# Optimization experiments

Measured on AMD Instinct MI355X. Metric: run time of the kernel, lower is better.

Reference implementation:

```python
import jax, jax.numpy as jnp
import numpy as np

B, S, D, H, E = 64, 1024, 1024, 64, 8  # batch, seq, model_dim, bottleneck, num_adapters
EPS = 1e-5


def setup_inputs() -> dict:
    key = jax.random.key(0)
    ks = jax.random.split(key, 8)
    x = jax.random.normal(ks[0], (B, S, D), jnp.float32)
    return {
        "x": x,
        # pre-adapter LayerNorm params
        "ln_g": jnp.ones((D,), jnp.float32),
        "ln_b": jnp.zeros((D,), jnp.float32),
        # router BatchNorm1d (eval mode: running stats)
        "bn_g": jnp.ones((D,), jnp.float32),
        "bn_b": jnp.zeros((D,), jnp.float32),
        "bn_mean": jax.random.normal(ks[1], (D,), jnp.float32) * 0.01,
        "bn_var": jnp.ones((D,), jnp.float32),
        # router linear D -> E
        "Wr": jax.random.normal(ks[2], (D, E), jnp.float32) * 0.02,
        "br": jnp.zeros((E,), jnp.float32),
        # per-expert bottleneck adapter weights
        "W_down": jax.random.normal(ks[3], (E, D, H), jnp.float32) * 0.02,
        "b_down": jnp.zeros((E, H), jnp.float32),
        "W_up": jax.random.normal(ks[4], (E, H, D), jnp.float32) * 0.02,
        "b_up": jnp.zeros((E, D), jnp.float32),
    }


def reference(x, ln_g, ln_b, bn_g, bn_b, bn_mean, bn_var, Wr, br,
              W_down, b_down, W_up, b_up):
    # pre layer norm
    mu = jnp.mean(x, axis=-1, keepdims=True)
    var = jnp.var(x, axis=-1, keepdims=True)
    z = (x - mu) * jax.lax.rsqrt(var + EPS) * ln_g + ln_b  # [B,S,D]

    # sentence embedding -> batchnorm (eval) -> router softmax
    z_sent = jnp.mean(z, axis=1)  # [B,D]
    z_bn = (z_sent - bn_mean) * jax.lax.rsqrt(bn_var + EPS) * bn_g + bn_b
    probs = jax.nn.softmax(z_bn @ Wr + br, axis=-1)  # [B,E]

    # hard top-1 routing; gate = prob of selected expert (SparseDispatcher combine)
    idx = jnp.argmax(probs, axis=-1)  # [B] int
    gate = jnp.take_along_axis(probs, idx[:, None], axis=1)[:, 0]  # [B]

    # per-expert bottleneck adapter, applied via gathered expert weights
    # (mathematically identical to dispatch/per-expert-GEMM/scatter-combine)
    h = jax.nn.relu(jnp.einsum('bsd,bdh->bsh', z, W_down[idx]) + b_down[idx][:, None, :])
    y = jnp.einsum('bsh,bhd->bsd', h, W_up[idx]) + b_up[idx][:, None, :]

    return y * gate[:, None, None]  # weighted combine
```

## Files before the change

### kernel.cpp

```cpp
#include <hip/hip_runtime.h>
#include <hip/hip_bf16.h>

#define B_  64
#define S_  1024
#define D_  1024
#define H_  64
#define E_  8
#define EPS_ 1e-5f

typedef __attribute__((ext_vector_type(8))) __bf16 bf16x8;
typedef __attribute__((ext_vector_type(4))) __bf16 bf16x4;
typedef __attribute__((ext_vector_type(4))) float f32x4;

__global__ __launch_bounds__(256) void swz_kernel(
    const float* __restrict__ Wd, const float* __restrict__ Wu,
    __bf16* __restrict__ wd_swz, __bf16* __restrict__ wu_swz)
{
    int t = blockIdx.x * 256 + threadIdx.x;
    if (t < 65536) {
        int e = t >> 13, rem = t & 8191;
        int ks = rem >> 8, nc = (rem >> 6) & 3, lane = rem & 63;
        int k0 = ks * 32 + (lane >> 4) * 8, n = nc * 16 + (lane & 15);
        bf16x8 o;
#pragma unroll
        for (int j = 0; j < 8; ++j)
            o[j] = (__bf16)Wd[((size_t)e * D_ + k0 + j) * H_ + n];
        *(bf16x8*)(wd_swz + (size_t)t * 8) = o;
    } else {
        int t2 = t - 65536;
        int e = t2 >> 13, rem = t2 & 8191;
        int ks = rem >> 12, nc = (rem >> 6) & 63, lane = rem & 63;
        int k0 = ks * 32 + (lane >> 4) * 8, n = nc * 16 + (lane & 15);
        bf16x8 o;
#pragma unroll
        for (int j = 0; j < 8; ++j)
            o[j] = (__bf16)Wu[((size_t)e * H_ + k0 + j) * D_ + n];
        *(bf16x8*)(wu_swz + (size_t)t2 * 8) = o;
    }
}

__global__ __launch_bounds__(256) void ln_kernel(
    const float* __restrict__ x, const float* __restrict__ ln_g,
    const float* __restrict__ ln_b,
    __bf16* __restrict__ z, float* __restrict__ zpart)
{
    const int lane = threadIdx.x & 63, w = threadIdx.x >> 6;
    const int b = blockIdx.x >> 5, sblk = blockIdx.x & 31;
    __shared__ float accs[D_];
    for (int i = threadIdx.x; i < D_; i += 256) accs[i] = 0.f;
    __syncthreads();

    float part[16];
#pragma unroll
    for (int i = 0; i < 16; ++i) part[i] = 0.f;

    for (int it = 0; it < 8; ++it) {
        int s = sblk * 32 + it * 4 + w;
        const float* xr = x + ((size_t)b * S_ + s) * D_;
        f32x4 v[4];
        float s1 = 0.f, s2 = 0.f;
#pragma unroll
        for (int j = 0; j < 4; ++j) {
            v[j] = *(const f32x4*)(xr + j * 256 + lane * 4);
#pragma unroll
            for (int tt = 0; tt < 4; ++tt) { s1 += v[j][tt]; s2 += v[j][tt] * v[j][tt]; }
        }
#pragma unroll
        for (int o = 32; o; o >>= 1) { s1 += __shfl_xor(s1, o); s2 += __shfl_xor(s2, o); }
        float mu = s1 * (1.f / D_);
        float var = s2 * (1.f / D_) - mu * mu;
        float rs = rsqrtf(var + EPS_);

        __bf16 zb[16];
#pragma unroll
        for (int j = 0; j < 4; ++j) {
            int c0 = j * 256 + lane * 4;
            f32x4 gg = *(const f32x4*)(ln_g + c0);
            f32x4 bb = *(const f32x4*)(ln_b + c0);
#pragma unroll
            for (int tt = 0; tt < 4; ++tt) {
                float zz = (v[j][tt] - mu) * rs * gg[tt] + bb[tt];
                part[j * 4 + tt] += zz;
                zb[j * 4 + tt] = (__bf16)zz;
            }
        }
        __bf16* zr = z + ((size_t)b * S_ + s) * D_;
#pragma unroll
        for (int j = 0; j < 4; ++j)
            *(bf16x4*)(zr + j * 256 + lane * 4) = *(bf16x4*)&zb[j * 4];
    }

#pragma unroll
    for (int j = 0; j < 4; ++j)
#pragma unroll
        for (int tt = 0; tt < 4; ++tt)
            atomicAdd(&accs[j * 256 + lane * 4 + tt], part[j * 4 + tt]);
    __syncthreads();
    float* zp = zpart + ((size_t)b * 32 + sblk) * D_;
    for (int i = threadIdx.x; i < D_; i += 256) zp[i] = accs[i];
}

__global__ __launch_bounds__(256) void router_kernel(
    const float* __restrict__ zpart,
    const float* __restrict__ bn_g, const float* __restrict__ bn_b,
    const float* __restrict__ bn_mean, const float* __restrict__ bn_var,
    const float* __restrict__ Wr, const float* __restrict__ br,
    int* __restrict__ idx, float* __restrict__ gate)
{
    const int b = blockIdx.x, tid = threadIdx.x;
    float acc[E_] = {};
    for (int d = tid; d < D_; d += 256) {
        float s = 0.f;
#pragma unroll
        for (int p = 0; p < 32; ++p) s += zpart[((size_t)b * 32 + p) * D_ + d];
        float zb = (s * (1.f / S_) - bn_mean[d]) * rsqrtf(bn_var[d] + EPS_) * bn_g[d] + bn_b[d];
#pragma unroll
        for (int e = 0; e < E_; ++e) acc[e] += zb * Wr[d * E_ + e];
    }
#pragma unroll
    for (int o = 32; o; o >>= 1)
#pragma unroll
        for (int e = 0; e < E_; ++e) acc[e] += __shfl_xor(acc[e], o);

    __shared__ float red[4][E_];
    int lane = tid & 63, w = tid >> 6;
    if (lane == 0)
#pragma unroll
        for (int e = 0; e < E_; ++e) red[w][e] = acc[e];
    __syncthreads();
    if (tid == 0) {
        float logits[E_];
#pragma unroll
        for (int e = 0; e < E_; ++e)
            logits[e] = red[0][e] + red[1][e] + red[2][e] + red[3][e] + br[e];
        float mx = logits[0]; int am = 0;
#pragma unroll
        for (int e = 1; e < E_; ++e) if (logits[e] > mx) { mx = logits[e]; am = e; }
        float den = 0.f;
#pragma unroll
        for (int e = 0; e < E_; ++e) den += expf(logits[e] - mx);
        idx[b] = am;
        gate[b] = 1.f / den;
    }
}

__global__ __launch_bounds__(256) void adapter_kernel(
    const __bf16* __restrict__ z, const __bf16* __restrict__ wd_swz,
    const __bf16* __restrict__ wu_swz,
    const float* __restrict__ b_down, const float* __restrict__ b_up,
    const int* __restrict__ idx, const float* __restrict__ gate,
    float* __restrict__ out)
{
    const int tid = threadIdx.x, lane = tid & 63, w = tid >> 6;
    const int b = blockIdx.x >> 3, tile = blockIdx.x & 7;
    const int e = idx[b];
    const float g = gate[b];
    const int s0 = tile * 128 + w * 32;
    const int r = lane & 15, kb = lane >> 4;

    f32x4 acc[2][4] = {};
    const __bf16* zrow0 = z + ((size_t)(b * S_ + s0 + r)) * D_ + kb * 8;
    const __bf16* zrow1 = zrow0 + (size_t)16 * D_;
    const __bf16* wdp = wd_swz + ((size_t)e * 32 * 4 * 64 + lane) * 8;
#pragma unroll 4
    for (int ks = 0; ks < 32; ++ks) {
        bf16x8 a0 = *(const bf16x8*)(zrow0 + ks * 32);
        bf16x8 a1 = *(const bf16x8*)(zrow1 + ks * 32);
        const __bf16* wk = wdp + (size_t)ks * (4 * 64 * 8);
#pragma unroll
        for (int nc = 0; nc < 4; ++nc) {
            bf16x8 bf = *(const bf16x8*)(wk + nc * (64 * 8));
            acc[0][nc] = __builtin_amdgcn_mfma_f32_16x16x32_bf16(a0, bf, acc[0][nc], 0, 0, 0);
            acc[1][nc] = __builtin_amdgcn_mfma_f32_16x16x32_bf16(a1, bf, acc[1][nc], 0, 0, 0);
        }
    }

    __shared__ __bf16 hlds[4][32 * 64];
    __bf16* hw = &hlds[w][0];
#pragma unroll
    for (int mr = 0; mr < 2; ++mr)
#pragma unroll
        for (int nc = 0; nc < 4; ++nc)
#pragma unroll
            for (int reg = 0; reg < 4; ++reg) {
                int row = mr * 16 + kb * 4 + reg;
                int col = nc * 16 + r;
                float v = acc[mr][nc][reg] + b_down[e * H_ + col];
                v = fmaxf(v, 0.f);
                int chunk = (col >> 3) ^ (row & 7);
                hw[row * 64 + chunk * 8 + (col & 7)] = (__bf16)v;
            }
    __syncthreads();

    bf16x8 a2[2][2];
#pragma unroll
    for (int mr = 0; mr < 2; ++mr)
#pragma unroll
        for (int ks2 = 0; ks2 < 2; ++ks2) {
            int row = mr * 16 + r;
            int chunk = (ks2 * 4 + kb) ^ (row & 7);
            a2[mr][ks2] = *(const bf16x8*)(hw + row * 64 + chunk * 8);
        }

    const __bf16* wup = wu_swz + ((size_t)e * 2 * 64 * 64 + lane) * 8;
    float* outp = out + ((size_t)(b * S_ + s0)) * D_;
#pragma unroll 2
    for (int nc2 = 0; nc2 < 64; ++nc2) {
        bf16x8 b0 = *(const bf16x8*)(wup + (size_t)(0 * 64 + nc2) * (64 * 8));
        bf16x8 b1 = *(const bf16x8*)(wup + (size_t)(1 * 64 + nc2) * (64 * 8));
        int d = nc2 * 16 + r;
        float bup = b_up[e * D_ + d];
#pragma unroll
        for (int mr = 0; mr < 2; ++mr) {
            f32x4 acy = {};
            acy = __builtin_amdgcn_mfma_f32_16x16x32_bf16(a2[mr][0], b0, acy, 0, 0, 0);
            acy = __builtin_amdgcn_mfma_f32_16x16x32_bf16(a2[mr][1], b1, acy, 0, 0, 0);
#pragma unroll
            for (int reg = 0; reg < 4; ++reg) {
                int row = mr * 16 + kb * 4 + reg;
                outp[(size_t)row * D_ + d] = (acy[reg] + bup) * g;
            }
        }
    }
}

extern "C" void kernel_launch(void* const* d_in, const int* in_sizes, int n_in,
                              void* d_out, int out_size, void* d_ws, size_t ws_size,
                              hipStream_t stream)
{
    const float* x       = (const float*)d_in[0];
    const float* ln_g    = (const float*)d_in[1];
    const float* ln_b    = (const float*)d_in[2];
    const float* bn_g    = (const float*)d_in[3];
    const float* bn_b    = (const float*)d_in[4];
    const float* bn_mean = (const float*)d_in[5];
    const float* bn_var  = (const float*)d_in[6];
    const float* Wr      = (const float*)d_in[7];
    const float* br      = (const float*)d_in[8];
    const float* W_down  = (const float*)d_in[9];
    const float* b_down  = (const float*)d_in[10];
    const float* W_up    = (const float*)d_in[11];
    const float* b_up    = (const float*)d_in[12];
    float* out = (float*)d_out;

    char* ws = (char*)d_ws;
    __bf16* z       = (__bf16*)(ws);
    float*  zpart   = (float*)(ws + 134217728);
    __bf16* wd_swz  = (__bf16*)(ws + 142606336);
    __bf16* wu_swz  = (__bf16*)(ws + 143654912);
    int*    idx     = (int*)(ws + 144703488);
    float*  gate    = (float*)(ws + 144703744);

    swz_kernel<<<dim3(512), dim3(256), 0, stream>>>(W_down, W_up, wd_swz, wu_swz);
    ln_kernel<<<dim3(B_ * 32), dim3(256), 0, stream>>>(x, ln_g, ln_b, z, zpart);
    router_kernel<<<dim3(B_), dim3(256), 0, stream>>>(zpart, bn_g, bn_b, bn_mean,
                                                      bn_var, Wr, br, idx, gate);
    adapter_kernel<<<dim3(B_ * 8), dim3(256), 0, stream>>>(z, wd_swz, wu_swz,
                                                           b_down, b_up, idx, gate, out);
}
```

Measured before the change: 606.3 us.

## Split adapter into down and up kernels with transposed MFMA for vectorized stores

Splits the fused adapter kernel into a down-projection kernel that writes the bf16 bottleneck activations h to global memory, and an up-projection kernel with twice as many blocks. The MFMA operands are swapped (weights as A, activations as B) so each lane holds four consecutive output columns and can issue 16-byte float4 stores instead of scattered scalar stores. The LayerNorm kernel also doubles its grid, with the router summing 64 partial sums instead of 32. This costs an extra launch and a round trip of h (about 8 MB) through global memory.

```diff
diff --git a/kernel.cpp b/kernel.cpp
--- a/kernel.cpp
+++ b/kernel.cpp
@@ -45,7 +45,7 @@
     __bf16* __restrict__ z, float* __restrict__ zpart)
 {
     const int lane = threadIdx.x & 63, w = threadIdx.x >> 6;
-    const int b = blockIdx.x >> 5, sblk = blockIdx.x & 31;
+    const int b = blockIdx.x >> 6, sblk = blockIdx.x & 63;
     __shared__ float accs[D_];
     for (int i = threadIdx.x; i < D_; i += 256) accs[i] = 0.f;
     __syncthreads();
@@ -54,8 +54,8 @@
 #pragma unroll
     for (int i = 0; i < 16; ++i) part[i] = 0.f;
 
-    for (int it = 0; it < 8; ++it) {
-        int s = sblk * 32 + it * 4 + w;
+    for (int it = 0; it < 4; ++it) {
+        int s = sblk * 16 + it * 4 + w;
         const float* xr = x + ((size_t)b * S_ + s) * D_;
         f32x4 v[4];
         float s1 = 0.f, s2 = 0.f;
@@ -96,7 +96,7 @@
         for (int tt = 0; tt < 4; ++tt)
             atomicAdd(&accs[j * 256 + lane * 4 + tt], part[j * 4 + tt]);
     __syncthreads();
-    float* zp = zpart + ((size_t)b * 32 + sblk) * D_;
+    float* zp = zpart + ((size_t)b * 64 + sblk) * D_;
     for (int i = threadIdx.x; i < D_; i += 256) zp[i] = accs[i];
 }
 
@@ -112,7 +112,7 @@
     for (int d = tid; d < D_; d += 256) {
         float s = 0.f;
 #pragma unroll
-        for (int p = 0; p < 32; ++p) s += zpart[((size_t)b * 32 + p) * D_ + d];
+        for (int p = 0; p < 64; ++p) s += zpart[((size_t)b * 64 + p) * D_ + d];
         float zb = (s * (1.f / S_) - bn_mean[d]) * rsqrtf(bn_var[d] + EPS_) * bn_g[d] + bn_b[d];
 #pragma unroll
         for (int e = 0; e < E_; ++e) acc[e] += zb * Wr[d * E_ + e];
@@ -144,83 +144,78 @@
     }
 }
 
-__global__ __launch_bounds__(256) void adapter_kernel(
+__global__ __launch_bounds__(256) void down_kernel(
     const __bf16* __restrict__ z, const __bf16* __restrict__ wd_swz,
-    const __bf16* __restrict__ wu_swz,
-    const float* __restrict__ b_down, const float* __restrict__ b_up,
-    const int* __restrict__ idx, const float* __restrict__ gate,
-    float* __restrict__ out)
+    const float* __restrict__ b_down, const int* __restrict__ idx,
+    __bf16* __restrict__ h)
 {
     const int tid = threadIdx.x, lane = tid & 63, w = tid >> 6;
     const int b = blockIdx.x >> 3, tile = blockIdx.x & 7;
     const int e = idx[b];
-    const float g = gate[b];
     const int s0 = tile * 128 + w * 32;
     const int r = lane & 15, kb = lane >> 4;
 
     f32x4 acc[2][4] = {};
-    const __bf16* zrow0 = z + ((size_t)(b * S_ + s0 + r)) * D_ + kb * 8;
-    const __bf16* zrow1 = zrow0 + (size_t)16 * D_;
+    const __bf16* z0 = z + ((size_t)(b * S_ + s0 + r)) * D_ + kb * 8;
+    const __bf16* z1 = z0 + (size_t)16 * D_;
     const __bf16* wdp = wd_swz + ((size_t)e * 32 * 4 * 64 + lane) * 8;
 #pragma unroll 4
     for (int ks = 0; ks < 32; ++ks) {
-        bf16x8 a0 = *(const bf16x8*)(zrow0 + ks * 32);
-        bf16x8 a1 = *(const bf16x8*)(zrow1 + ks * 32);
+        bf16x8 zb0 = *(const bf16x8*)(z0 + ks * 32);
+        bf16x8 zb1 = *(const bf16x8*)(z1 + ks * 32);
         const __bf16* wk = wdp + (size_t)ks * (4 * 64 * 8);
 #pragma unroll
-        for (int nc = 0; nc < 4; ++nc) {
-            bf16x8 bf = *(const bf16x8*)(wk + nc * (64 * 8));
-            acc[0][nc] = __builtin_amdgcn_mfma_f32_16x16x32_bf16(a0, bf, acc[0][nc], 0, 0, 0);
-            acc[1][nc] = __builtin_amdgcn_mfma_f32_16x16x32_bf16(a1, bf, acc[1][nc], 0, 0, 0);
-        }
-    }
-
-    __shared__ __bf16 hlds[4][32 * 64];
-    __bf16* hw = &hlds[w][0];
-#pragma unroll
-    for (int mr = 0; mr < 2; ++mr)
-#pragma unroll
-        for (int nc = 0; nc < 4; ++nc)
-#pragma unroll
-            for (int reg = 0; reg < 4; ++reg) {
-                int row = mr * 16 + kb * 4 + reg;
-                int col = nc * 16 + r;
-                float v = acc[mr][nc][reg] + b_down[e * H_ + col];
-                v = fmaxf(v, 0.f);
-                int chunk = (col >> 3) ^ (row & 7);
-                hw[row * 64 + chunk * 8 + (col & 7)] = (__bf16)v;
-            }
-    __syncthreads();
-
-    bf16x8 a2[2][2];
-#pragma unroll
-    for (int mr = 0; mr < 2; ++mr)
-#pragma unroll
-        for (int ks2 = 0; ks2 < 2; ++ks2) {
-            int row = mr * 16 + r;
-            int chunk = (ks2 * 4 + kb) ^ (row & 7);
-            a2[mr][ks2] = *(const bf16x8*)(hw + row * 64 + chunk * 8);
-        }
-
+        for (int ht = 0; ht < 4; ++ht) {
+            bf16x8 a = *(const bf16x8*)(wk + ht * (64 * 8));
+            acc[0][ht] = __builtin_amdgcn_mfma_f32_16x16x32_bf16(a, zb0, acc[0][ht], 0, 0, 0);
+            acc[1][ht] = __builtin_amdgcn_mfma_f32_16x16x32_bf16(a, zb1, acc[1][ht], 0, 0, 0);
+        }
+    }
+
+#pragma unroll
+    for (int st = 0; st < 2; ++st)
+#pragma unroll
+        for (int ht = 0; ht < 4; ++ht) {
+            f32x4 bd = *(const f32x4*)(b_down + e * H_ + ht * 16 + kb * 4);
+            bf16x4 hv;
+#pragma unroll
+            for (int reg = 0; reg < 4; ++reg)
+                hv[reg] = (__bf16)fmaxf(acc[st][ht][reg] + bd[reg], 0.f);
+            *(bf16x4*)(h + ((size_t)(b * S_ + s0 + st * 16 + r)) * H_ + ht * 16 + kb * 4) = hv;
+        }
+}
+
+__global__ __launch_bounds__(256) void up_kernel(
+    const __bf16* __restrict__ h, const __bf16* __restrict__ wu_swz,
+    const float* __restrict__ b_up, const int* __restrict__ idx,
+    const float* __restrict__ gate, float* __restrict__ out)
+{
+    const int tid = threadIdx.x, lane = tid & 63, w = tid >> 6;
+    const int b = blockIdx.x >> 4, tile = blockIdx.x & 15;
+    const int e = idx[b];
+    const float g = gate[b];
+    const int s0 = tile * 64 + w * 16;
+    const int r = lane & 15, kb = lane >> 4;
+
+    const __bf16* hrow = h + ((size_t)(b * S_ + s0 + r)) * H_ + kb * 8;
+    bf16x8 hb0 = *(const bf16x8*)(hrow);
+    bf16x8 hb1 = *(const bf16x8*)(hrow + 32);
     const __bf16* wup = wu_swz + ((size_t)e * 2 * 64 * 64 + lane) * 8;
-    float* outp = out + ((size_t)(b * S_ + s0)) * D_;
-#pragma unroll 2
-    for (int nc2 = 0; nc2 < 64; ++nc2) {
-        bf16x8 b0 = *(const bf16x8*)(wup + (size_t)(0 * 64 + nc2) * (64 * 8));
-        bf16x8 b1 = *(const bf16x8*)(wup + (size_t)(1 * 64 + nc2) * (64 * 8));
-        int d = nc2 * 16 + r;
-        float bup = b_up[e * D_ + d];
-#pragma unroll
-        for (int mr = 0; mr < 2; ++mr) {
-            f32x4 acy = {};
-            acy = __builtin_amdgcn_mfma_f32_16x16x32_bf16(a2[mr][0], b0, acy, 0, 0, 0);
-            acy = __builtin_amdgcn_mfma_f32_16x16x32_bf16(a2[mr][1], b1, acy, 0, 0, 0);
-#pragma unroll
-            for (int reg = 0; reg < 4; ++reg) {
-                int row = mr * 16 + kb * 4 + reg;
-                outp[(size_t)row * D_ + d] = (acy[reg] + bup) * g;
-            }
-        }
+    float* orow = out + ((size_t)(b * S_ + s0 + r)) * D_ + kb * 4;
+    const float* bup = b_up + e * D_ + kb * 4;
+
+#pragma unroll 4
+    for (int dt = 0; dt < 64; ++dt) {
+        bf16x8 a0 = *(const bf16x8*)(wup + (size_t)dt * (64 * 8));
+        bf16x8 a1 = *(const bf16x8*)(wup + (size_t)(64 * 64 * 8) + (size_t)dt * (64 * 8));
+        f32x4 acy = {};
+        acy = __builtin_amdgcn_mfma_f32_16x16x32_bf16(a0, hb0, acy, 0, 0, 0);
+        acy = __builtin_amdgcn_mfma_f32_16x16x32_bf16(a1, hb1, acy, 0, 0, 0);
+        f32x4 bv = *(const f32x4*)(bup + dt * 16);
+        f32x4 o;
+#pragma unroll
+        for (int reg = 0; reg < 4; ++reg) o[reg] = (acy[reg] + bv[reg]) * g;
+        *(f32x4*)(orow + dt * 16) = o;
     }
 }
 
@@ -246,15 +241,16 @@
     char* ws = (char*)d_ws;
     __bf16* z       = (__bf16*)(ws);
     float*  zpart   = (float*)(ws + 134217728);
-    __bf16* wd_swz  = (__bf16*)(ws + 142606336);
-    __bf16* wu_swz  = (__bf16*)(ws + 143654912);
-    int*    idx     = (int*)(ws + 144703488);
-    float*  gate    = (float*)(ws + 144703744);
+    __bf16* h       = (__bf16*)(ws + 150994944);
+    __bf16* wd_swz  = (__bf16*)(ws + 159383552);
+    __bf16* wu_swz  = (__bf16*)(ws + 160432128);
+    int*    idx     = (int*)(ws + 161480704);
+    float*  gate    = (float*)(ws + 161480960);
 
     swz_kernel<<<dim3(512), dim3(256), 0, stream>>>(W_down, W_up, wd_swz, wu_swz);
-    ln_kernel<<<dim3(B_ * 32), dim3(256), 0, stream>>>(x, ln_g, ln_b, z, zpart);
+    ln_kernel<<<dim3(B_ * 64), dim3(256), 0, stream>>>(x, ln_g, ln_b, z, zpart);
     router_kernel<<<dim3(B_), dim3(256), 0, stream>>>(zpart, bn_g, bn_b, bn_mean,
                                                       bn_var, Wr, br, idx, gate);
-    adapter_kernel<<<dim3(B_ * 8), dim3(256), 0, stream>>>(z, wd_swz, wu_swz,
-                                                           b_down, b_up, idx, gate, out);
-}
+    down_kernel<<<dim3(B_ * 8), dim3(256), 0, stream>>>(z, wd_swz, b_down, idx, h);
+    up_kernel<<<dim3(B_ * 16), dim3(256), 0, stream>>>(h, wu_swz, b_up, idx, gate, out);
+}
```

New measurement: 629.6 us. +3.8%, slower.
